# Performance work log

Measured on AMD Instinct MI355X. Metric: run time of the kernel, lower is better.

The kernel has to match this reference:

```python
import jax, jax.numpy as jnp
import numpy as np

N_NODES = 100000
N_EDGES = 1600000
NODE_IN = 32
HID = 64
EDGE_IN = 8


def _glorot(key, shape):
    fan_in = shape[0]
    return jax.random.normal(key, shape, jnp.float32) * (1.0 / np.sqrt(fan_in))


def setup_inputs() -> dict:
    key = jax.random.key(0)
    ks = jax.random.split(key, 16)
    d = {}
    d["x"] = jax.random.normal(ks[0], (N_NODES, NODE_IN), jnp.float32)
    d["edge_index"] = jax.random.randint(ks[1], (2, N_EDGES), 0, N_NODES, dtype=jnp.int32)
    d["edge_attr"] = jax.random.normal(ks[2], (N_EDGES, EDGE_IN), jnp.float32)
    # SAGEConv layers: lin_l (aggregated neighbors, with bias), lin_r (root, no bias)
    d["Wl0"] = _glorot(ks[3], (NODE_IN, HID)); d["bl0"] = jnp.zeros((HID,), jnp.float32)
    d["Wr0"] = _glorot(ks[4], (NODE_IN, HID))
    d["Wl1"] = _glorot(ks[5], (HID, HID)); d["bl1"] = jnp.zeros((HID,), jnp.float32)
    d["Wr1"] = _glorot(ks[6], (HID, HID))
    d["Wl2"] = _glorot(ks[7], (HID, HID)); d["bl2"] = jnp.zeros((HID,), jnp.float32)
    d["Wr2"] = _glorot(ks[8], (HID, HID))
    # Edge predictor MLP: (2*HID + EDGE_IN) -> 64 -> 32 -> 1
    pin = 2 * HID + EDGE_IN
    d["W1"] = _glorot(ks[9], (pin, 64)); d["b1"] = jnp.zeros((64,), jnp.float32)
    d["W2"] = _glorot(ks[10], (64, 32)); d["b2"] = jnp.zeros((32,), jnp.float32)
    d["W3"] = _glorot(ks[11], (32, 1)); d["b3"] = jnp.zeros((1,), jnp.float32)
    return d


def _sage_mean(h, src, dst, Wl, bl, Wr):
    # PyG SAGEConv(aggr='mean'): lin_l(mean_{j->i} x_j) + lin_r(x_i)
    n = h.shape[0]
    summed = jax.ops.segment_sum(h[src], dst, num_segments=n)  # [N, F]
    cnt = jax.ops.segment_sum(jnp.ones((src.shape[0], 1), h.dtype), dst, num_segments=n)
    mean = summed / jnp.maximum(cnt, 1.0)
    return mean @ Wl + bl + h @ Wr


def reference(x, edge_index, edge_attr,
              Wl0, bl0, Wr0, Wl1, bl1, Wr1, Wl2, bl2, Wr2,
              W1, b1, W2, b2, W3, b3):
    src, dst = edge_index[0], edge_index[1]
    h = _sage_mean(x, src, dst, Wl0, bl0, Wr0)
    h = jax.nn.relu(h)  # dropout inactive (eval mode)
    h = _sage_mean(h, src, dst, Wl1, bl1, Wr1)
    h = jax.nn.relu(h)
    h = _sage_mean(h, src, dst, Wl2, bl2, Wr2)
    # Edge-level predictor: gather endpoint embeddings + edge features
    edge_repr = jnp.concatenate([h[src], h[dst], edge_attr], axis=1)  # [E, 2*HID+EDGE_IN]
    z = jax.nn.relu(edge_repr @ W1 + b1)
    z = jax.nn.relu(z @ W2 + b2)
    return jax.nn.sigmoid(z @ W3 + b3)  # [E, 1]
```

## Files before the change

kernel.cpp:

```cpp
#include <hip/hip_runtime.h>
#include <hip/hip_bf16.h>

#define NN 100000
#define NE 1600000
#define HID 64
#define SCAN_BS 256
#define NBLK ((NN + SCAN_BS - 1) / SCAN_BS)

typedef float f32x4 __attribute__((ext_vector_type(4)));
typedef short bf16x8 __attribute__((ext_vector_type(8)));

__device__ __forceinline__ float bflo(unsigned u) { return __uint_as_float(u << 16); }
__device__ __forceinline__ float bfhi(unsigned u) { return __uint_as_float(u & 0xffff0000u); }
__device__ __forceinline__ unsigned short f2bf(float f) {
    __hip_bfloat16 h = (__hip_bfloat16)f;
    return *(unsigned short*)&h;
}

__global__ void xcast(const float* __restrict__ in, unsigned short* __restrict__ out, int n4) {
    int i = blockIdx.x * blockDim.x + threadIdx.x;
    if (i >= n4) return;
    float4 v = ((const float4*)in)[i];
    ushort4 o;
    o.x = f2bf(v.x); o.y = f2bf(v.y); o.z = f2bf(v.z); o.w = f2bf(v.w);
    ((ushort4*)out)[i] = o;
}

__global__ void count_kernel(const int* __restrict__ dst, int* __restrict__ degI, int nE) {
    int e = blockIdx.x * blockDim.x + threadIdx.x;
    if (e < nE) atomicAdd(&degI[dst[e]], 1);
}

__global__ void scan1_kernel(const int* __restrict__ degI, int* __restrict__ rowtmp,
                             int* __restrict__ blockSum) {
    __shared__ int tmp[SCAN_BS];
    int t = threadIdx.x;
    int i = blockIdx.x * SCAN_BS + t;
    int d = (i < NN) ? degI[i] : 0;
    tmp[t] = d;
    __syncthreads();
    for (int off = 1; off < SCAN_BS; off <<= 1) {
        int v = (t >= off) ? tmp[t - off] : 0;
        __syncthreads();
        tmp[t] += v;
        __syncthreads();
    }
    if (i < NN) rowtmp[i] = tmp[t] - d;
    if (t == SCAN_BS - 1) blockSum[blockIdx.x] = tmp[t];
}

__global__ void scan2_kernel(const int* __restrict__ blockSum, int* __restrict__ blockOff, int n) {
    __shared__ int tmp[512];
    int t = threadIdx.x;
    tmp[t] = (t < n) ? blockSum[t] : 0;
    __syncthreads();
    for (int off = 1; off < 512; off <<= 1) {
        int v = (t >= off) ? tmp[t - off] : 0;
        __syncthreads();
        tmp[t] += v;
        __syncthreads();
    }
    if (t < n) blockOff[t] = (t == 0) ? 0 : tmp[t - 1];
}

__global__ void scan3_kernel(const int* __restrict__ rowtmp, const int* __restrict__ blockOff,
                             int* __restrict__ row_ptr) {
    int i = blockIdx.x * SCAN_BS + threadIdx.x;
    if (i < NN) row_ptr[i] = rowtmp[i] + blockOff[blockIdx.x];
}

__global__ void fill_kernel(const int* __restrict__ src, const int* __restrict__ dst,
                            const int* __restrict__ row_ptr, int* __restrict__ cursor,
                            int* __restrict__ csr_src, int nE) {
    int e = blockIdx.x * blockDim.x + threadIdx.x;
    if (e >= nE) return;
    int d = dst[e];
    int pos = atomicAdd(&cursor[d], 1);
    csr_src[row_ptr[d] + pos] = src[e];
}

template <int IN>
__launch_bounds__(256)
__global__ void aggregate(const int* __restrict__ row_ptr, const int* __restrict__ degI,
                          const int* __restrict__ csr_src,
                          const unsigned short* __restrict__ hin,
                          float* __restrict__ mout) {
    constexpr int LPE = IN / 4;
    constexpr int SPLIT = 64 / LPE;
    constexpr int UN = (SPLIT >= 8) ? 2 : 4;
    int g = threadIdx.x >> 6;
    int lane = threadIdx.x & 63;
    int node = blockIdx.x * 4 + g;
    int lane_p = lane & (LPE - 1);
    int sub = lane / LPE;

    float a0 = 0.f, a1 = 0.f, a2 = 0.f, a3 = 0.f;
    int start = row_ptr[node];
    int dg = degI[node];
    const int* cs = csr_src + start;

    int e = sub;
    for (; e + SPLIT * (UN - 1) < dg; e += SPLIT * UN) {
        int sidx[UN];
#pragma unroll
        for (int j = 0; j < UN; ++j) sidx[j] = cs[e + SPLIT * j];
        uint2 u[UN];
#pragma unroll
        for (int j = 0; j < UN; ++j)
            u[j] = *(const uint2*)(hin + (size_t)sidx[j] * IN + 4 * lane_p);
#pragma unroll
        for (int j = 0; j < UN; ++j) {
            a0 += bflo(u[j].x); a1 += bfhi(u[j].x);
            a2 += bflo(u[j].y); a3 += bfhi(u[j].y);
        }
    }
    for (; e < dg; e += SPLIT) {
        uint2 u = *(const uint2*)(hin + (size_t)cs[e] * IN + 4 * lane_p);
        a0 += bflo(u.x); a1 += bfhi(u.x);
        a2 += bflo(u.y); a3 += bfhi(u.y);
    }

#pragma unroll
    for (int m = LPE; m < 64; m <<= 1) {
        a0 += __shfl_xor(a0, m);
        a1 += __shfl_xor(a1, m);
        a2 += __shfl_xor(a2, m);
        a3 += __shfl_xor(a3, m);
    }
    if (sub == 0) {
        float r = 1.0f / fmaxf((float)dg, 1.0f);
        float4 v;
        v.x = a0 * r; v.y = a1 * r; v.z = a2 * r; v.w = a3 * r;
        *(float4*)(mout + (size_t)node * IN + 4 * lane_p) = v;
    }
}

__global__ void wprep(const float* __restrict__ Wl0, const float* __restrict__ Wr0,
                      const float* __restrict__ Wl1, const float* __restrict__ Wr1,
                      const float* __restrict__ Wl2, const float* __restrict__ Wr2,
                      const float* __restrict__ W1, unsigned short* __restrict__ out) {
    int b = blockIdx.x;
    int mid, local;
    if (b < 2) { mid = b; local = 0; }
    else { mid = 2 + (b - 2) / 2; local = (b - 2) & 1; }
    const float* Ws[8] = {Wl0, Wr0, Wl1, Wr1, Wl2, Wr2, W1, W1 + 64 * 64};
    const int offs[8] = {0, 4096, 8192, 16384, 24576, 32768, 40960, 49152};
    const float* W = Ws[mid];
    int e = local * 256 + threadIdx.x;
    int lane = e & 63;
    int fi = e >> 6;
    int ks = fi >> 2, nt = fi & 3;
    int lg = lane >> 4, col = lane & 15;
    unsigned short hi[8], lo[8];
#pragma unroll
    for (int j = 0; j < 8; ++j) {
        float w = W[(ks * 32 + lg * 8 + j) * 64 + nt * 16 + col];
        unsigned short h = f2bf(w);
        hi[j] = h;
        lo[j] = f2bf(w - bflo(h));
    }
    unsigned short* dh = out + offs[mid] + ((size_t)(fi * 2 + 0) * 64 + lane) * 8;
    unsigned short* dl = out + offs[mid] + ((size_t)(fi * 2 + 1) * 64 + lane) * 8;
#pragma unroll
    for (int j = 0; j < 8; ++j) { dh[j] = hi[j]; dl[j] = lo[j]; }
}

__global__ void wprep2(const float* __restrict__ W1, const float* __restrict__ b1,
                       const float* __restrict__ W2, const float* __restrict__ b2,
                       unsigned short* __restrict__ we_pk,
                       unsigned short* __restrict__ w2h_pk,
                       unsigned short* __restrict__ w2l_pk) {
    int t = threadIdx.x;
    const float* W1e = W1 + 128 * 64;
    {
        int mt = t >> 6, lane = t & 63;
        int ar = lane & 15, lg = lane >> 4;
        int f = mt * 16 + ar;
        unsigned short v[8];
#pragma unroll
        for (int j = 0; j < 8; ++j) {
            if (lg <= 1) {
                v[j] = f2bf(W1e[j * 64 + f]);
            } else if (lg == 2) {
                float w = W1e[j * 64 + f];
                unsigned short h = f2bf(w);
                v[j] = f2bf(w - bflo(h));
            } else {
                if (j == 0) v[j] = f2bf(b1[f]);
                else if (j == 1) {
                    float bb = b1[f];
                    unsigned short h = f2bf(bb);
                    v[j] = f2bf(bb - bflo(h));
                } else v[j] = 0;
            }
        }
        unsigned short* o = we_pk + (size_t)t * 8;
        for (int j = 0; j < 8; ++j) o[j] = v[j];
    }
    for (int i = t; i < 640; i += 256) {
        int mt2 = i / 320, rem = i % 320;
        int ks = rem >> 6, lane = rem & 63;
        int ar = lane & 15, lg = lane >> 4;
        int c = mt2 * 16 + ar;
        unsigned short v[8] = {0, 0, 0, 0, 0, 0, 0, 0};
        if (ks < 4) {
            for (int j = 0; j < 4; ++j)
                v[j] = f2bf(W2[(ks * 16 + lg * 4 + j) * 32 + c]);
        } else if (lg == 0) {
            float bb = b2[c];
            unsigned short h = f2bf(bb);
            v[0] = h;
            v[1] = f2bf(bb - bflo(h));
        }
        unsigned short* o = w2h_pk + (size_t)i * 8;
        for (int j = 0; j < 8; ++j) o[j] = v[j];
    }
    for (int i = t; i < 512; i += 256) {
        int mt2 = i / 256, rem = i % 256;
        int ks = rem >> 6, lane = rem & 63;
        int ar = lane & 15, lg = lane >> 4;
        int c = mt2 * 16 + ar;
        unsigned short v[8] = {0, 0, 0, 0, 0, 0, 0, 0};
        for (int j = 0; j < 4; ++j) {
            float w = W2[(ks * 16 + lg * 4 + j) * 32 + c];
            unsigned short h = f2bf(w);
            v[j] = f2bf(w - bflo(h));
        }
        unsigned short* o = w2l_pk + (size_t)i * 8;
        for (int j = 0; j < 8; ++j) o[j] = v[j];
    }
}

template <int KIN, bool RELU>
__launch_bounds__(256)
__global__ void sage_gemm(const float* __restrict__ meanv,
                          const unsigned short* __restrict__ hroot,
                          const unsigned short* __restrict__ wl_pk,
                          const unsigned short* __restrict__ wr_pk,
                          const float* __restrict__ bl,
                          unsigned short* __restrict__ hout) {
    constexpr int NKS = KIN / 32;
    int wid = threadIdx.x >> 6, lane = threadIdx.x & 63;
    int tile = blockIdx.x * 4 + wid;
    if (tile >= NN / 16) return;
    int m0 = tile * 16;
    int ar = lane & 15;
    int lg = lane >> 4;

    bf16x8 ah[NKS];
#pragma unroll
    for (int ks = 0; ks < NKS; ++ks)
        ah[ks] = *(const bf16x8*)(hroot + (size_t)(m0 + ar) * KIN + ks * 32 + lg * 8);

    bf16x8 amh[NKS], aml[NKS];
#pragma unroll
    for (int ks = 0; ks < NKS; ++ks) {
        const float* p = meanv + (size_t)(m0 + ar) * KIN + ks * 32 + lg * 8;
        float4 v0 = *(const float4*)p;
        float4 v1 = *(const float4*)(p + 4);
        float mv[8] = {v0.x, v0.y, v0.z, v0.w, v1.x, v1.y, v1.z, v1.w};
#pragma unroll
        for (int j = 0; j < 8; ++j) {
            unsigned short h = f2bf(mv[j]);
            amh[ks][j] = (short)h;
            aml[ks][j] = (short)f2bf(mv[j] - bflo(h));
        }
    }

#pragma unroll
    for (int nt = 0; nt < 4; ++nt) {
        f32x4 acc = {0.f, 0.f, 0.f, 0.f};
#pragma unroll
        for (int ks = 0; ks < NKS; ++ks) {
            int fi = ks * 4 + nt;
            bf16x8 wlh = *(const bf16x8*)(wl_pk + ((size_t)(fi * 2 + 0) * 64 + lane) * 8);
            bf16x8 wll = *(const bf16x8*)(wl_pk + ((size_t)(fi * 2 + 1) * 64 + lane) * 8);
            bf16x8 wrh = *(const bf16x8*)(wr_pk + ((size_t)(fi * 2 + 0) * 64 + lane) * 8);
            bf16x8 wrl = *(const bf16x8*)(wr_pk + ((size_t)(fi * 2 + 1) * 64 + lane) * 8);
            acc = __builtin_amdgcn_mfma_f32_16x16x32_bf16(amh[ks], wlh, acc, 0, 0, 0);
            acc = __builtin_amdgcn_mfma_f32_16x16x32_bf16(amh[ks], wll, acc, 0, 0, 0);
            acc = __builtin_amdgcn_mfma_f32_16x16x32_bf16(aml[ks], wlh, acc, 0, 0, 0);
            acc = __builtin_amdgcn_mfma_f32_16x16x32_bf16(ah[ks],  wrh, acc, 0, 0, 0);
            acc = __builtin_amdgcn_mfma_f32_16x16x32_bf16(ah[ks],  wrl, acc, 0, 0, 0);
        }
        float b = bl[nt * 16 + ar];
#pragma unroll
        for (int r = 0; r < 4; ++r) {
            float o = acc[r] + b;
            if (RELU) o = fmaxf(o, 0.f);
            hout[(size_t)(m0 + lg * 4 + r) * 64 + nt * 16 + ar] = f2bf(o);
        }
    }
}

__launch_bounds__(256)
__global__ void pred_gemm(const unsigned short* __restrict__ h2,
                          const unsigned short* __restrict__ wa_pk,
                          const unsigned short* __restrict__ wb_pk,
                          unsigned short* __restrict__ a1,
                          unsigned short* __restrict__ a2) {
    int wid = threadIdx.x >> 6, lane = threadIdx.x & 63;
    int tile = blockIdx.x * 4 + wid;
    if (tile >= NN / 16) return;
    int m0 = tile * 16;
    int ar = lane & 15;
    int lg = lane >> 4;
    bf16x8 ah[2];
#pragma unroll
    for (int ks = 0; ks < 2; ++ks)
        ah[ks] = *(const bf16x8*)(h2 + (size_t)(m0 + ar) * 64 + ks * 32 + lg * 8);
#pragma unroll
    for (int nt = 0; nt < 4; ++nt) {
        f32x4 p = {0.f, 0.f, 0.f, 0.f};
        f32x4 q = {0.f, 0.f, 0.f, 0.f};
#pragma unroll
        for (int ks = 0; ks < 2; ++ks) {
            int fi = ks * 4 + nt;
            bf16x8 wah = *(const bf16x8*)(wa_pk + ((size_t)(fi * 2 + 0) * 64 + lane) * 8);
            bf16x8 wal = *(const bf16x8*)(wa_pk + ((size_t)(fi * 2 + 1) * 64 + lane) * 8);
            bf16x8 wbh = *(const bf16x8*)(wb_pk + ((size_t)(fi * 2 + 0) * 64 + lane) * 8);
            bf16x8 wbl = *(const bf16x8*)(wb_pk + ((size_t)(fi * 2 + 1) * 64 + lane) * 8);
            p = __builtin_amdgcn_mfma_f32_16x16x32_bf16(ah[ks], wah, p, 0, 0, 0);
            p = __builtin_amdgcn_mfma_f32_16x16x32_bf16(ah[ks], wal, p, 0, 0, 0);
            q = __builtin_amdgcn_mfma_f32_16x16x32_bf16(ah[ks], wbh, q, 0, 0, 0);
            q = __builtin_amdgcn_mfma_f32_16x16x32_bf16(ah[ks], wbl, q, 0, 0, 0);
        }
#pragma unroll
        for (int r = 0; r < 4; ++r) {
            size_t off = (size_t)(m0 + lg * 4 + r) * 64 + nt * 16 + ar;
            a1[off] = f2bf(p[r]);
            a2[off] = f2bf(q[r]);
        }
    }
}

__launch_bounds__(256)
__global__ void edge_pred(const int* __restrict__ src, const int* __restrict__ dst,
                          const unsigned short* __restrict__ a1, const unsigned short* __restrict__ a2,
                          const float* __restrict__ ea,
                          const unsigned short* __restrict__ we_pk,
                          const unsigned short* __restrict__ w2h_pk,
                          const unsigned short* __restrict__ w2l_pk,
                          const float* __restrict__ W3, const float* __restrict__ b3,
                          float* __restrict__ out) {
    int wid = threadIdx.x >> 6, lane = threadIdx.x & 63;
    int tile = blockIdx.x * 4 + wid;
    int e0 = tile * 16;
    int ar = lane & 15, lg = lane >> 4;
    int e = e0 + ar;

    int s = src[e];
    int d = dst[e];

    const float4* ep = (const float4*)(ea + (size_t)e * 8);
    float4 f0 = ep[0], f1 = ep[1];
    float ev[8] = {f0.x, f0.y, f0.z, f0.w, f1.x, f1.y, f1.z, f1.w};
    bf16x8 bea = {0, 0, 0, 0, 0, 0, 0, 0};
    if (lg == 3) {
        bea[0] = (short)0x3F80; bea[1] = (short)0x3F80;
    } else if (lg == 1) {
#pragma unroll
        for (int j = 0; j < 8; ++j) {
            unsigned short h = f2bf(ev[j]);
            bea[j] = (short)f2bf(ev[j] - bflo(h));
        }
    } else {
#pragma unroll
        for (int j = 0; j < 8; ++j) bea[j] = (short)f2bf(ev[j]);
    }

    uint2 ua[4], ub[4];
#pragma unroll
    for (int ks = 0; ks < 4; ++ks) {
        ua[ks] = *(const uint2*)(a1 + (size_t)s * 64 + ks * 16 + lg * 4);
        ub[ks] = *(const uint2*)(a2 + (size_t)d * 64 + ks * 16 + lg * 4);
    }

    f32x4 accE[4];
#pragma unroll
    for (int mt = 0; mt < 4; ++mt) {
        bf16x8 aw = *(const bf16x8*)(we_pk + ((size_t)(mt * 64 + lane)) * 8);
        f32x4 z = {0.f, 0.f, 0.f, 0.f};
        accE[mt] = __builtin_amdgcn_mfma_f32_16x16x32_bf16(aw, bea, z, 0, 0, 0);
    }

    f32x4 acc2[2] = {{0.f, 0.f, 0.f, 0.f}, {0.f, 0.f, 0.f, 0.f}};
#pragma unroll
    for (int ks = 0; ks < 4; ++ks) {
        float z0 = accE[ks][0] + bflo(ua[ks].x) + bflo(ub[ks].x);
        float z1 = accE[ks][1] + bfhi(ua[ks].x) + bfhi(ub[ks].x);
        float z2 = accE[ks][2] + bflo(ua[ks].y) + bflo(ub[ks].y);
        float z3 = accE[ks][3] + bfhi(ua[ks].y) + bfhi(ub[ks].y);
        z0 = fmaxf(z0, 0.f); z1 = fmaxf(z1, 0.f);
        z2 = fmaxf(z2, 0.f); z3 = fmaxf(z3, 0.f);
        unsigned short h0 = f2bf(z0), h1 = f2bf(z1), h2 = f2bf(z2), h3 = f2bf(z3);
        bf16x8 zh = {(short)h0, (short)h1, (short)h2, (short)h3, 0, 0, 0, 0};
        bf16x8 zl = {(short)f2bf(z0 - bflo(h0)), (short)f2bf(z1 - bflo(h1)),
                     (short)f2bf(z2 - bflo(h2)), (short)f2bf(z3 - bflo(h3)), 0, 0, 0, 0};
#pragma unroll
        for (int mt2 = 0; mt2 < 2; ++mt2) {
            bf16x8 Ah = *(const bf16x8*)(w2h_pk + ((size_t)((mt2 * 5 + ks) * 64 + lane)) * 8);
            bf16x8 Al = *(const bf16x8*)(w2l_pk + ((size_t)((mt2 * 4 + ks) * 64 + lane)) * 8);
            acc2[mt2] = __builtin_amdgcn_mfma_f32_16x16x32_bf16(Ah, zh, acc2[mt2], 0, 0, 0);
            acc2[mt2] = __builtin_amdgcn_mfma_f32_16x16x32_bf16(Ah, zl, acc2[mt2], 0, 0, 0);
            acc2[mt2] = __builtin_amdgcn_mfma_f32_16x16x32_bf16(Al, zh, acc2[mt2], 0, 0, 0);
        }
    }
    {
        bf16x8 bone = {0, 0, 0, 0, 0, 0, 0, 0};
        if (lg == 0) { bone[0] = (short)0x3F80; bone[1] = (short)0x3F80; }
#pragma unroll
        for (int mt2 = 0; mt2 < 2; ++mt2) {
            bf16x8 Ah = *(const bf16x8*)(w2h_pk + ((size_t)((mt2 * 5 + 4) * 64 + lane)) * 8);
            acc2[mt2] = __builtin_amdgcn_mfma_f32_16x16x32_bf16(Ah, bone, acc2[mt2], 0, 0, 0);
        }
    }

    float p = 0.f;
#pragma unroll
    for (int mt2 = 0; mt2 < 2; ++mt2) {
        float4 w3 = *(const float4*)(W3 + mt2 * 16 + lg * 4);
        p = fmaf(fmaxf(acc2[mt2][0], 0.f), w3.x, p);
        p = fmaf(fmaxf(acc2[mt2][1], 0.f), w3.y, p);
        p = fmaf(fmaxf(acc2[mt2][2], 0.f), w3.z, p);
        p = fmaf(fmaxf(acc2[mt2][3], 0.f), w3.w, p);
    }
    p += __shfl_xor(p, 16);
    p += __shfl_xor(p, 32);
    if (lane < 16) {
        float o = p + b3[0];
        out[e] = 1.0f / (1.0f + __expf(-o));
    }
}

extern "C" void kernel_launch(void* const* d_in, const int* in_sizes, int n_in,
                              void* d_out, int out_size, void* d_ws, size_t ws_size,
                              hipStream_t stream) {
    const float* x   = (const float*)d_in[0];
    const int*   ei  = (const int*)d_in[1];
    const float* ea  = (const float*)d_in[2];
    const float* Wl0 = (const float*)d_in[3];
    const float* bl0 = (const float*)d_in[4];
    const float* Wr0 = (const float*)d_in[5];
    const float* Wl1 = (const float*)d_in[6];
    const float* bl1 = (const float*)d_in[7];
    const float* Wr1 = (const float*)d_in[8];
    const float* Wl2 = (const float*)d_in[9];
    const float* bl2 = (const float*)d_in[10];
    const float* Wr2 = (const float*)d_in[11];
    const float* W1  = (const float*)d_in[12];
    const float* b1  = (const float*)d_in[13];
    const float* W2  = (const float*)d_in[14];
    const float* b2  = (const float*)d_in[15];
    const float* W3  = (const float*)d_in[16];
    const float* b3  = (const float*)d_in[17];

    const int* src = ei;
    const int* dst = ei + NE;

    char* ws = (char*)d_ws;
    size_t off = 0;
    auto alloc = [&](size_t bytes) {
        void* p = ws + off;
        off += (bytes + 255) & ~(size_t)255;
        return p;
    };
    unsigned short* xb = (unsigned short*)alloc((size_t)NN * 32 * 2);
    unsigned short* hA = (unsigned short*)alloc((size_t)NN * HID * 2);
    unsigned short* hB = (unsigned short*)alloc((size_t)NN * HID * 2);
    unsigned short* a1 = (unsigned short*)alloc((size_t)NN * HID * 2);
    unsigned short* a2 = (unsigned short*)alloc((size_t)NN * HID * 2);
    unsigned short* wpk = (unsigned short*)alloc((size_t)68608 * 2);
    int* degI    = (int*)alloc(NN * sizeof(int));
    int* row_ptr = (int*)alloc(NN * sizeof(int));
    int* rowtmp  = (int*)alloc(NN * sizeof(int));
    int* cursor  = (int*)alloc(NN * sizeof(int));
    int* blockSum= (int*)alloc(512 * sizeof(int));
    int* blockOff= (int*)alloc(512 * sizeof(int));
    int* csr_src = (int*)alloc((size_t)NE * sizeof(int));
    float* meanv = (float*)a1;
    float* out = (float*)d_out;

    unsigned short* we_pk  = wpk + 57344;
    unsigned short* w2h_pk = wpk + 59392;
    unsigned short* w2l_pk = wpk + 64512;

    const int BS = 256;
    dim3 blkE((NE + BS - 1) / BS);
    int n4 = NN * 32 / 4;
    int gemm_blk = (NN / 16 + 3) / 4;

    hipMemsetAsync(degI, 0, NN * sizeof(int), stream);
    hipMemsetAsync(cursor, 0, NN * sizeof(int), stream);
    xcast<<<(n4 + BS - 1) / BS, BS, 0, stream>>>(x, xb, n4);
    count_kernel<<<blkE, BS, 0, stream>>>(dst, degI, NE);
    scan1_kernel<<<NBLK, SCAN_BS, 0, stream>>>(degI, rowtmp, blockSum);
    scan2_kernel<<<1, 512, 0, stream>>>(blockSum, blockOff, NBLK);
    scan3_kernel<<<NBLK, SCAN_BS, 0, stream>>>(rowtmp, blockOff, row_ptr);
    fill_kernel<<<blkE, BS, 0, stream>>>(src, dst, row_ptr, cursor, csr_src, NE);
    wprep<<<14, 256, 0, stream>>>(Wl0, Wr0, Wl1, Wr1, Wl2, Wr2, W1, wpk);
    wprep2<<<1, 256, 0, stream>>>(W1, b1, W2, b2, we_pk, w2h_pk, w2l_pk);

    aggregate<32><<<NN / 4, 256, 0, stream>>>(row_ptr, degI, csr_src, xb, meanv);
    sage_gemm<32, true><<<gemm_blk, 256, 0, stream>>>(meanv, xb, wpk + 0, wpk + 4096, bl0, hA);
    aggregate<64><<<NN / 4, 256, 0, stream>>>(row_ptr, degI, csr_src, hA, meanv);
    sage_gemm<64, true><<<gemm_blk, 256, 0, stream>>>(meanv, hA, wpk + 8192, wpk + 16384, bl1, hB);
    aggregate<64><<<NN / 4, 256, 0, stream>>>(row_ptr, degI, csr_src, hB, meanv);
    sage_gemm<64, false><<<gemm_blk, 256, 0, stream>>>(meanv, hB, wpk + 24576, wpk + 32768, bl2, hA);
    pred_gemm<<<gemm_blk, 256, 0, stream>>>(hA, wpk + 40960, wpk + 49152, a1, a2);

    edge_pred<<<NE / 64, BS, 0, stream>>>(src, dst, a1, a2, ea, we_pk, w2h_pk, w2l_pk, W3, b3, out);
}
```

Baseline: 633.1 us.

## Process four edge tiles per wave in edge_pred with batched gathers

Each wave now handles four 16-edge tiles. It issues all index, endpoint-embedding and edge-feature loads up front so more memory requests are in flight, and it loads the first-layer weights once for all tiles. The b2 bias is added directly in the epilogue, which replaces the extra MFMA that multiplied against a ones vector. In exchange the kernel holds more live registers, which may lower occupancy, and it launches a quarter as many blocks.

Measured after the change: 631.7 us. No clear change (-0.2%).

```diff
diff --git a/kernel.cpp b/kernel.cpp
--- a/kernel.cpp
+++ b/kernel.cpp
@@ -342,94 +342,117 @@
                           const unsigned short* __restrict__ w2h_pk,
                           const unsigned short* __restrict__ w2l_pk,
                           const float* __restrict__ W3, const float* __restrict__ b3,
+                          const float* __restrict__ b2,
                           float* __restrict__ out) {
+    constexpr int TPW = 4;
     int wid = threadIdx.x >> 6, lane = threadIdx.x & 63;
-    int tile = blockIdx.x * 4 + wid;
-    int e0 = tile * 16;
     int ar = lane & 15, lg = lane >> 4;
-    int e = e0 + ar;
-
-    int s = src[e];
-    int d = dst[e];
-
-    const float4* ep = (const float4*)(ea + (size_t)e * 8);
-    float4 f0 = ep[0], f1 = ep[1];
-    float ev[8] = {f0.x, f0.y, f0.z, f0.w, f1.x, f1.y, f1.z, f1.w};
-    bf16x8 bea = {0, 0, 0, 0, 0, 0, 0, 0};
-    if (lg == 3) {
-        bea[0] = (short)0x3F80; bea[1] = (short)0x3F80;
-    } else if (lg == 1) {
-#pragma unroll
-        for (int j = 0; j < 8; ++j) {
-            unsigned short h = f2bf(ev[j]);
-            bea[j] = (short)f2bf(ev[j] - bflo(h));
-        }
-    } else {
-#pragma unroll
-        for (int j = 0; j < 8; ++j) bea[j] = (short)f2bf(ev[j]);
-    }
-
-    uint2 ua[4], ub[4];
-#pragma unroll
-    for (int ks = 0; ks < 4; ++ks) {
-        ua[ks] = *(const uint2*)(a1 + (size_t)s * 64 + ks * 16 + lg * 4);
-        ub[ks] = *(const uint2*)(a2 + (size_t)d * 64 + ks * 16 + lg * 4);
-    }
-
-    f32x4 accE[4];
-#pragma unroll
-    for (int mt = 0; mt < 4; ++mt) {
-        bf16x8 aw = *(const bf16x8*)(we_pk + ((size_t)(mt * 64 + lane)) * 8);
-        f32x4 z = {0.f, 0.f, 0.f, 0.f};
-        accE[mt] = __builtin_amdgcn_mfma_f32_16x16x32_bf16(aw, bea, z, 0, 0, 0);
-    }
-
-    f32x4 acc2[2] = {{0.f, 0.f, 0.f, 0.f}, {0.f, 0.f, 0.f, 0.f}};
-#pragma unroll
-    for (int ks = 0; ks < 4; ++ks) {
-        float z0 = accE[ks][0] + bflo(ua[ks].x) + bflo(ub[ks].x);
-        float z1 = accE[ks][1] + bfhi(ua[ks].x) + bfhi(ub[ks].x);
-        float z2 = accE[ks][2] + bflo(ua[ks].y) + bflo(ub[ks].y);
-        float z3 = accE[ks][3] + bfhi(ua[ks].y) + bfhi(ub[ks].y);
-        z0 = fmaxf(z0, 0.f); z1 = fmaxf(z1, 0.f);
-        z2 = fmaxf(z2, 0.f); z3 = fmaxf(z3, 0.f);
-        unsigned short h0 = f2bf(z0), h1 = f2bf(z1), h2 = f2bf(z2), h3 = f2bf(z3);
-        bf16x8 zh = {(short)h0, (short)h1, (short)h2, (short)h3, 0, 0, 0, 0};
-        bf16x8 zl = {(short)f2bf(z0 - bflo(h0)), (short)f2bf(z1 - bflo(h1)),
-                     (short)f2bf(z2 - bflo(h2)), (short)f2bf(z3 - bflo(h3)), 0, 0, 0, 0};
-#pragma unroll
-        for (int mt2 = 0; mt2 < 2; ++mt2) {
-            bf16x8 Ah = *(const bf16x8*)(w2h_pk + ((size_t)((mt2 * 5 + ks) * 64 + lane)) * 8);
-            bf16x8 Al = *(const bf16x8*)(w2l_pk + ((size_t)((mt2 * 4 + ks) * 64 + lane)) * 8);
-            acc2[mt2] = __builtin_amdgcn_mfma_f32_16x16x32_bf16(Ah, zh, acc2[mt2], 0, 0, 0);
-            acc2[mt2] = __builtin_amdgcn_mfma_f32_16x16x32_bf16(Ah, zl, acc2[mt2], 0, 0, 0);
-            acc2[mt2] = __builtin_amdgcn_mfma_f32_16x16x32_bf16(Al, zh, acc2[mt2], 0, 0, 0);
-        }
-    }
-    {
-        bf16x8 bone = {0, 0, 0, 0, 0, 0, 0, 0};
-        if (lg == 0) { bone[0] = (short)0x3F80; bone[1] = (short)0x3F80; }
-#pragma unroll
-        for (int mt2 = 0; mt2 < 2; ++mt2) {
-            bf16x8 Ah = *(const bf16x8*)(w2h_pk + ((size_t)((mt2 * 5 + 4) * 64 + lane)) * 8);
-            acc2[mt2] = __builtin_amdgcn_mfma_f32_16x16x32_bf16(Ah, bone, acc2[mt2], 0, 0, 0);
-        }
-    }
-
-    float p = 0.f;
-#pragma unroll
-    for (int mt2 = 0; mt2 < 2; ++mt2) {
-        float4 w3 = *(const float4*)(W3 + mt2 * 16 + lg * 4);
-        p = fmaf(fmaxf(acc2[mt2][0], 0.f), w3.x, p);
-        p = fmaf(fmaxf(acc2[mt2][1], 0.f), w3.y, p);
-        p = fmaf(fmaxf(acc2[mt2][2], 0.f), w3.z, p);
-        p = fmaf(fmaxf(acc2[mt2][3], 0.f), w3.w, p);
-    }
-    p += __shfl_xor(p, 16);
-    p += __shfl_xor(p, 32);
-    if (lane < 16) {
-        float o = p + b3[0];
-        out[e] = 1.0f / (1.0f + __expf(-o));
+    int tile0 = (blockIdx.x * 4 + wid) * TPW;
+
+    int ei_[TPW], s_[TPW], d_[TPW];
+#pragma unroll
+    for (int t = 0; t < TPW; ++t) {
+        int e = (tile0 + t) * 16 + ar;
+        ei_[t] = e;
+        s_[t] = src[e];
+        d_[t] = dst[e];
+    }
+    uint2 ua[TPW][4], ub[TPW][4];
+#pragma unroll
+    for (int t = 0; t < TPW; ++t) {
+        const unsigned short* pa = a1 + (size_t)s_[t] * 64 + lg * 4;
+        const unsigned short* pb = a2 + (size_t)d_[t] * 64 + lg * 4;
+#pragma unroll
+        for (int ks = 0; ks < 4; ++ks) {
+            ua[t][ks] = *(const uint2*)(pa + ks * 16);
+            ub[t][ks] = *(const uint2*)(pb + ks * 16);
+        }
+    }
+    float4 ef0[TPW], ef1[TPW];
+#pragma unroll
+    for (int t = 0; t < TPW; ++t) {
+        const float4* ep = (const float4*)(ea + (size_t)ei_[t] * 8);
+        ef0[t] = ep[0];
+        ef1[t] = ep[1];
+    }
+
+    bf16x8 aw[4];
+#pragma unroll
+    for (int mt = 0; mt < 4; ++mt)
+        aw[mt] = *(const bf16x8*)(we_pk + ((size_t)(mt * 64 + lane)) * 8);
+    float4 b2v0 = *(const float4*)(b2 + lg * 4);
+    float4 b2v1 = *(const float4*)(b2 + 16 + lg * 4);
+    float4 w3a = *(const float4*)(W3 + lg * 4);
+    float4 w3b = *(const float4*)(W3 + 16 + lg * 4);
+
+    float pz[TPW];
+#pragma unroll
+    for (int t = 0; t < TPW; ++t) {
+        float evv[8] = {ef0[t].x, ef0[t].y, ef0[t].z, ef0[t].w,
+                        ef1[t].x, ef1[t].y, ef1[t].z, ef1[t].w};
+        bf16x8 bea = {0, 0, 0, 0, 0, 0, 0, 0};
+        if (lg == 3) {
+            bea[0] = (short)0x3F80; bea[1] = (short)0x3F80;
+        } else if (lg == 1) {
+#pragma unroll
+            for (int j = 0; j < 8; ++j) {
+                unsigned short h = f2bf(evv[j]);
+                bea[j] = (short)f2bf(evv[j] - bflo(h));
+            }
+        } else {
+#pragma unroll
+            for (int j = 0; j < 8; ++j) bea[j] = (short)f2bf(evv[j]);
+        }
+
+        f32x4 accE[4];
+#pragma unroll
+        for (int mt = 0; mt < 4; ++mt) {
+            f32x4 z = {0.f, 0.f, 0.f, 0.f};
+            accE[mt] = __builtin_amdgcn_mfma_f32_16x16x32_bf16(aw[mt], bea, z, 0, 0, 0);
+        }
+
+        f32x4 acc2[2] = {{0.f, 0.f, 0.f, 0.f}, {0.f, 0.f, 0.f, 0.f}};
+#pragma unroll
+        for (int ks = 0; ks < 4; ++ks) {
+            float z0 = accE[ks][0] + bflo(ua[t][ks].x) + bflo(ub[t][ks].x);
+            float z1 = accE[ks][1] + bfhi(ua[t][ks].x) + bfhi(ub[t][ks].x);
+            float z2 = accE[ks][2] + bflo(ua[t][ks].y) + bflo(ub[t][ks].y);
+            float z3 = accE[ks][3] + bfhi(ua[t][ks].y) + bfhi(ub[t][ks].y);
+            z0 = fmaxf(z0, 0.f); z1 = fmaxf(z1, 0.f);
+            z2 = fmaxf(z2, 0.f); z3 = fmaxf(z3, 0.f);
+            unsigned short h0 = f2bf(z0), h1 = f2bf(z1), h2 = f2bf(z2), h3 = f2bf(z3);
+            bf16x8 zh = {(short)h0, (short)h1, (short)h2, (short)h3, 0, 0, 0, 0};
+            bf16x8 zl = {(short)f2bf(z0 - bflo(h0)), (short)f2bf(z1 - bflo(h1)),
+                         (short)f2bf(z2 - bflo(h2)), (short)f2bf(z3 - bflo(h3)), 0, 0, 0, 0};
+#pragma unroll
+            for (int mt2 = 0; mt2 < 2; ++mt2) {
+                bf16x8 Ah = *(const bf16x8*)(w2h_pk + ((size_t)((mt2 * 5 + ks) * 64 + lane)) * 8);
+                bf16x8 Al = *(const bf16x8*)(w2l_pk + ((size_t)((mt2 * 4 + ks) * 64 + lane)) * 8);
+                acc2[mt2] = __builtin_amdgcn_mfma_f32_16x16x32_bf16(Ah, zh, acc2[mt2], 0, 0, 0);
+                acc2[mt2] = __builtin_amdgcn_mfma_f32_16x16x32_bf16(Ah, zl, acc2[mt2], 0, 0, 0);
+                acc2[mt2] = __builtin_amdgcn_mfma_f32_16x16x32_bf16(Al, zh, acc2[mt2], 0, 0, 0);
+            }
+        }
+
+        float p = 0.f;
+        p = fmaf(fmaxf(acc2[0][0] + b2v0.x, 0.f), w3a.x, p);
+        p = fmaf(fmaxf(acc2[0][1] + b2v0.y, 0.f), w3a.y, p);
+        p = fmaf(fmaxf(acc2[0][2] + b2v0.z, 0.f), w3a.z, p);
+        p = fmaf(fmaxf(acc2[0][3] + b2v0.w, 0.f), w3a.w, p);
+        p = fmaf(fmaxf(acc2[1][0] + b2v1.x, 0.f), w3b.x, p);
+        p = fmaf(fmaxf(acc2[1][1] + b2v1.y, 0.f), w3b.y, p);
+        p = fmaf(fmaxf(acc2[1][2] + b2v1.z, 0.f), w3b.z, p);
+        p = fmaf(fmaxf(acc2[1][3] + b2v1.w, 0.f), w3b.w, p);
+        p += __shfl_xor(p, 16);
+        p += __shfl_xor(p, 32);
+        pz[t] = p;
+    }
+
+    float bb3 = b3[0];
+#pragma unroll
+    for (int t = 0; t < TPW; ++t) {
+        if (lane < 16)
+            out[ei_[t]] = 1.0f / (1.0f + __expf(-(pz[t] + bb3)));
     }
 }
 
@@ -509,5 +532,5 @@
     sage_gemm<64, false><<<gemm_blk, 256, 0, stream>>>(meanv, hB, wpk + 24576, wpk + 32768, bl2, hA);
     pred_gemm<<<gemm_blk, 256, 0, stream>>>(hA, wpk + 40960, wpk + 49152, a1, a2);
 
-    edge_pred<<<NE / 64, BS, 0, stream>>>(src, dst, a1, a2, ea, we_pk, w2h_pk, w2l_pk, W3, b3, out);
-}
+    edge_pred<<<NE / 256, BS, 0, stream>>>(src, dst, a1, a2, ea, we_pk, w2h_pk, w2l_pk, W3, b3, b2, out);
+}
```
